# Performance work log

Hardware: AMD Instinct MI355X
Metric: run time of the kernel (lower is better)

Reference implementation:

```python
import jax, jax.numpy as jnp
import numpy as np
import math

B, T, F_ = 4, 1024, 1024
TO_DIM, FROM_DIM, LATENT, H = 1024, 1024, 1024, 16
HEAD_DIM = LATENT // H

def _linear_params(key, in_dim, out_dim):
    kw, kb = jax.random.split(key)
    bound = 1.0 / math.sqrt(in_dim)
    W = jax.random.uniform(kw, (out_dim, in_dim), minval=-bound, maxval=bound, dtype=jnp.float32)
    b = jax.random.uniform(kb, (out_dim,), minval=-bound, maxval=bound, dtype=jnp.float32)
    return W, b

def setup_inputs() -> dict:
    key = jax.random.key(0)
    ks = jax.random.split(key, 7)
    X_to = jax.random.normal(ks[0], (B, T, TO_DIM), dtype=jnp.float32)
    X_from = jax.random.normal(ks[1], (B, F_, FROM_DIM), dtype=jnp.float32)
    mask_from = jax.random.randint(ks[2], (B, T, F_), 0, 2, dtype=jnp.int32)
    Wq, bq = _linear_params(ks[3], TO_DIM, LATENT)
    Wk, bk = _linear_params(ks[4], FROM_DIM, LATENT)
    Wv, bv = _linear_params(ks[5], FROM_DIM, LATENT)
    Wo, bo = _linear_params(ks[6], LATENT, TO_DIM)
    return {"X_to": X_to, "X_from": X_from, "mask_from": mask_from,
            "Wq": Wq, "bq": bq, "Wk": Wk, "bk": bk, "Wv": Wv, "bv": bv, "Wo": Wo, "bo": bo}

def _split_heads(x):
    # [b, t, (h k)] -> [b, h, t, k]
    b, t, _ = x.shape
    return x.reshape(b, t, H, HEAD_DIM).transpose(0, 2, 1, 3)

def reference(X_to, X_from, mask_from, Wq, bq, Wk, bk, Wv, bv, Wo, bo):
    Q = _split_heads(X_to @ Wq.T + bq)
    # NOTE: source swaps names — K comes from v_linear, V from k_linear. Reproduced literally.
    K = _split_heads(X_from @ Wv.T + bv)
    V = _split_heads(X_from @ Wk.T + bk)
    attn = jnp.einsum('bhtk,bhfk->bhtf', Q, K) / math.sqrt(HEAD_DIM)
    attn = jnp.where(mask_from[:, None, :, :] == 0, jnp.float32(-10000.0), attn)
    attn = jax.nn.softmax(attn, axis=-1)
    out = jnp.einsum('bhtf,bhfk->bhtk', attn, V)  # [b,h,t,k]
    out = out.transpose(0, 2, 1, 3).reshape(X_to.shape[0], X_to.shape[1], LATENT)
    return out @ Wo.T + bo
```

## Files before the change

### kernel.cpp

```cpp
#include <hip/hip_runtime.h>
#include <hip/hip_bf16.h>
#include <math.h>

#define BB 4
#define TT 1024
#define FF 1024
#define DIM 1024
#define NH 16
#define HD 64
#define MROWS (BB * TT)
#define FB (FF / 64)

typedef __attribute__((ext_vector_type(8))) short short8;
typedef __attribute__((ext_vector_type(4))) float f32x4;
typedef __hip_bfloat16 bf16;

__device__ __forceinline__ void async_copy16(const void* g, void* l) {
    __builtin_amdgcn_global_load_lds((const __attribute__((address_space(1))) void*)g,
                                     (__attribute__((address_space(3))) void*)l,
                                     16, 0, 0);
}

struct ConvArgs {
    const float* src[6];
    bf16* dst[6];
    int nvec[6];
    int blk_end[6];
};

__global__ __launch_bounds__(256) void convert_batch(ConvArgs a) {
    int bx = blockIdx.x;
    int seg = 0;
#pragma unroll
    for (int k = 0; k < 5; ++k) if (bx >= a.blk_end[k]) seg = k + 1;
    int b0 = seg ? a.blk_end[seg - 1] : 0;
    int idx = (bx - b0) * 256 + threadIdx.x;
    if (idx >= a.nvec[seg]) return;
    float4 v = ((const float4*)a.src[seg])[idx];
    union { bf16 t[4]; ushort4 u; } o;
    o.t[0] = __float2bfloat16(v.x);
    o.t[1] = __float2bfloat16(v.y);
    o.t[2] = __float2bfloat16(v.z);
    o.t[3] = __float2bfloat16(v.w);
    *(ushort4*)(a.dst[seg] + 4 * (size_t)idx) = o.u;
}

__global__ __launch_bounds__(256) void mask_pack(const int* __restrict__ mask,
                                                 unsigned long long* __restrict__ Mb) {
    const int lane = threadIdx.x & 63;
    const int w = (blockIdx.x * 256 + threadIdx.x) >> 6;
    const int nw = (gridDim.x * 256) >> 6;
    const int NCH = BB * TT * FB;
    for (int c = w; c < NCH; c += nw) {
        int v = mask[(size_t)c * 64 + lane];
        unsigned long long bits = __ballot(v != 0);
        if (lane == 0) Mb[c] = bits;
    }
}

struct QkvArgs {
    const bf16* A[3]; const bf16* W[3]; const float* bias[3]; bf16* C[3];
    int N[3]; int biasRow[3];
};

__global__ __launch_bounds__(256) void gemm_qkv(QkvArgs q) {
    __shared__ bf16 As[128 * 32];
    __shared__ bf16 Bs[128 * 32];

    const int op = blockIdx.z;
    const bf16* A = q.A[op];
    const bf16* W = q.W[op];
    const float* bias = q.bias[op];
    bf16* C = q.C[op];
    const int N = q.N[op];
    const int brow = q.biasRow[op];

    int m0, n0;
    if (brow) { m0 = blockIdx.x * 128; n0 = blockIdx.y * 128; }
    else      { n0 = blockIdx.x * 128; m0 = blockIdx.y * 128; }

    const int tid  = threadIdx.x;
    const int lane = tid & 63;
    const int wave = tid >> 6;
    const int quad = lane >> 4;
    const int l16  = lane & 15;
    const int wm = wave & 1;
    const int wn = wave >> 1;
    const int wbase = tid & ~63;

    f32x4 acc[4][4] = {};

    for (int k0 = 0; k0 < DIM; k0 += 32) {
#pragma unroll
        for (int j = 0; j < 2; ++j) {
            int slot = j * 256 + tid;
            int r = slot >> 2;
            int blk = (slot & 3) ^ (r & 3);
            async_copy16(A + (size_t)(m0 + r) * DIM + k0 + blk * 8,
                         As + (size_t)(j * 256 + wbase) * 8);
            async_copy16(W + (size_t)(n0 + r) * DIM + k0 + blk * 8,
                         Bs + (size_t)(j * 256 + wbase) * 8);
        }
        __syncthreads();

        short8 a[4], b[4];
#pragma unroll
        for (int mi = 0; mi < 4; ++mi) {
            int r = wm * 64 + mi * 16 + l16;
            a[mi] = *(const short8*)(As + r * 32 + ((quad ^ (r & 3)) * 8));
        }
#pragma unroll
        for (int ni = 0; ni < 4; ++ni) {
            int r = wn * 64 + ni * 16 + l16;
            b[ni] = *(const short8*)(Bs + r * 32 + ((quad ^ (r & 3)) * 8));
        }
#pragma unroll
        for (int mi = 0; mi < 4; ++mi)
#pragma unroll
            for (int ni = 0; ni < 4; ++ni)
                acc[mi][ni] = __builtin_amdgcn_mfma_f32_16x16x32_bf16(
                    a[mi], b[ni], acc[mi][ni], 0, 0, 0);
        __syncthreads();
    }

#pragma unroll
    for (int ni = 0; ni < 4; ++ni) {
        const int n = n0 + wn * 64 + ni * 16 + l16;
        float bcol = brow ? 0.0f : bias[n];
#pragma unroll
        for (int mi = 0; mi < 4; ++mi) {
#pragma unroll
            for (int i = 0; i < 4; ++i) {
                const int m = m0 + wm * 64 + mi * 16 + quad * 4 + i;
                float v = acc[mi][ni][i] + (brow ? bias[m] : bcol);
                C[(size_t)m * N + n] = __float2bfloat16(v);
            }
        }
    }
}

__global__ __launch_bounds__(256) void gemm_o(
    const bf16* __restrict__ A, const bf16* __restrict__ W,
    const float* __restrict__ bias, float* __restrict__ C)
{
    __shared__ bf16 As[128 * 32];
    __shared__ bf16 Bs[64 * 32];

    const int n0 = blockIdx.x * 64;
    const int m0 = blockIdx.y * 128;
    const int tid  = threadIdx.x;
    const int lane = tid & 63;
    const int wave = tid >> 6;
    const int quad = lane >> 4;
    const int l16  = lane & 15;
    const int wm = wave & 1;
    const int wn = wave >> 1;
    const int wbase = tid & ~63;

    f32x4 acc[4][2] = {};

    for (int k0 = 0; k0 < DIM; k0 += 32) {
#pragma unroll
        for (int j = 0; j < 2; ++j) {
            int slot = j * 256 + tid;
            int r = slot >> 2;
            int blk = (slot & 3) ^ (r & 3);
            async_copy16(A + (size_t)(m0 + r) * DIM + k0 + blk * 8,
                         As + (size_t)(j * 256 + wbase) * 8);
        }
        {
            int r = tid >> 2;
            int blk = (tid & 3) ^ (r & 3);
            async_copy16(W + (size_t)(n0 + r) * DIM + k0 + blk * 8,
                         Bs + (size_t)wbase * 8);
        }
        __syncthreads();

        short8 a[4], b[2];
#pragma unroll
        for (int mi = 0; mi < 4; ++mi) {
            int r = wm * 64 + mi * 16 + l16;
            a[mi] = *(const short8*)(As + r * 32 + ((quad ^ (r & 3)) * 8));
        }
#pragma unroll
        for (int ni = 0; ni < 2; ++ni) {
            int r = wn * 32 + ni * 16 + l16;
            b[ni] = *(const short8*)(Bs + r * 32 + ((quad ^ (r & 3)) * 8));
        }
#pragma unroll
        for (int mi = 0; mi < 4; ++mi)
#pragma unroll
            for (int ni = 0; ni < 2; ++ni)
                acc[mi][ni] = __builtin_amdgcn_mfma_f32_16x16x32_bf16(
                    a[mi], b[ni], acc[mi][ni], 0, 0, 0);
        __syncthreads();
    }

#pragma unroll
    for (int ni = 0; ni < 2; ++ni) {
        const int n = n0 + wn * 32 + ni * 16 + l16;
        const float bcol = bias[n];
#pragma unroll
        for (int mi = 0; mi < 4; ++mi)
#pragma unroll
            for (int i = 0; i < 4; ++i) {
                const int m = m0 + wm * 64 + mi * 16 + quad * 4 + i;
                C[(size_t)m * DIM + n] = acc[mi][ni][i] + bcol;
            }
    }
}

__global__ __launch_bounds__(256) void attn_kernel(
    const bf16* Qg, const bf16* __restrict__ Kg, const bf16* __restrict__ Vtg,
    const unsigned long long* __restrict__ Mbits, bf16* Og)
{
    __shared__ bf16 Ks[64 * 64];
    __shared__ bf16 Vts[64 * 64];
    __shared__ bf16 Ps[64 * 72];

    const int tid  = threadIdx.x;
    const int lane = tid & 63;
    const int wave = tid >> 6;
    const int quad = lane >> 4;
    const int l16  = lane & 15;
    const int t0 = blockIdx.x * 64;
    const int h  = blockIdx.y;
    const int b  = blockIdx.z;
    const size_t qrow0 = (size_t)b * TT + t0;
    const size_t krow0 = (size_t)b * FF;
    const int wbase = tid & ~63;

    const bf16* qptr = Qg + (qrow0 + wave * 16 + l16) * DIM + h * HD;
    short8 qa0 = *(const short8*)(qptr + quad * 8);
    short8 qa1 = *(const short8*)(qptr + 32 + quad * 8);

    float lrow[4] = {0.f, 0.f, 0.f, 0.f};
    f32x4 oacc[4] = {};

    for (int f0 = 0; f0 < FF; f0 += 64) {
        const int fb = f0 >> 6;
#pragma unroll
        for (int j = 0; j < 2; ++j) {
            int slot = j * 256 + tid;
            int r = slot >> 3;
            int blk = (slot & 7) ^ (r & 7);
            async_copy16(Kg + (krow0 + f0 + r) * DIM + h * HD + blk * 8,
                         Ks + (size_t)(j * 256 + wbase) * 8);
            async_copy16(Vtg + (size_t)(h * HD + r) * MROWS + b * FF + f0 + blk * 8,
                         Vts + (size_t)(j * 256 + wbase) * 8);
        }
        __syncthreads();

        f32x4 sacc[4] = {};
#pragma unroll
        for (int nt = 0; nt < 4; ++nt) {
            int r = nt * 16 + l16;
            short8 kb0 = *(const short8*)(Ks + r * 64 + ((quad       ^ (r & 7)) * 8));
            short8 kb1 = *(const short8*)(Ks + r * 64 + (((quad + 4) ^ (r & 7)) * 8));
            sacc[nt] = __builtin_amdgcn_mfma_f32_16x16x32_bf16(qa0, kb0, sacc[nt], 0, 0, 0);
            sacc[nt] = __builtin_amdgcn_mfma_f32_16x16x32_bf16(qa1, kb1, sacc[nt], 0, 0, 0);
        }

#pragma unroll
        for (int i = 0; i < 4; ++i) {
            const int prow = wave * 16 + quad * 4 + i;
            unsigned long long m64 = Mbits[(qrow0 + prow) * FB + fb];
            unsigned long long sh = m64 >> l16;
            unsigned lo = (unsigned)sh, hi = (unsigned)(sh >> 32);
            float p0 = (lo & 1u)         ? __expf(sacc[0][i] * 0.125f) : 0.f;
            float p1 = ((lo >> 16) & 1u) ? __expf(sacc[1][i] * 0.125f) : 0.f;
            float p2 = (hi & 1u)         ? __expf(sacc[2][i] * 0.125f) : 0.f;
            float p3 = ((hi >> 16) & 1u) ? __expf(sacc[3][i] * 0.125f) : 0.f;
            lrow[i] += p0 + p1 + p2 + p3;
            Ps[prow * 72 +  0 + l16] = __float2bfloat16(p0);
            Ps[prow * 72 + 16 + l16] = __float2bfloat16(p1);
            Ps[prow * 72 + 32 + l16] = __float2bfloat16(p2);
            Ps[prow * 72 + 48 + l16] = __float2bfloat16(p3);
        }

        short8 pa0 = *(const short8*)(Ps + (wave * 16 + l16) * 72 + quad * 8);
        short8 pa1 = *(const short8*)(Ps + (wave * 16 + l16) * 72 + 32 + quad * 8);
#pragma unroll
        for (int nt = 0; nt < 4; ++nt) {
            int r = nt * 16 + l16;
            short8 vb0 = *(const short8*)(Vts + r * 64 + ((quad       ^ (r & 7)) * 8));
            short8 vb1 = *(const short8*)(Vts + r * 64 + (((quad + 4) ^ (r & 7)) * 8));
            oacc[nt] = __builtin_amdgcn_mfma_f32_16x16x32_bf16(pa0, vb0, oacc[nt], 0, 0, 0);
            oacc[nt] = __builtin_amdgcn_mfma_f32_16x16x32_bf16(pa1, vb1, oacc[nt], 0, 0, 0);
        }
        __syncthreads();
    }

#pragma unroll
    for (int i = 0; i < 4; ++i) {
        float l = lrow[i];
        l += __shfl_xor(l, 1);
        l += __shfl_xor(l, 2);
        l += __shfl_xor(l, 4);
        l += __shfl_xor(l, 8);
        float inv = 1.0f / l;
        const int prow = wave * 16 + quad * 4 + i;
#pragma unroll
        for (int nt = 0; nt < 4; ++nt)
            Ps[prow * 72 + nt * 16 + l16] = __float2bfloat16(oacc[nt][i] * inv);
    }
    __syncthreads();
#pragma unroll
    for (int j = 0; j < 2; ++j) {
        int s = j * 256 + tid;
        int rr = s >> 3, off = (s & 7) * 8;
        short8 v = *(const short8*)(Ps + rr * 72 + off);
        *(short8*)(Og + (qrow0 + rr) * DIM + h * HD + off) = v;
    }
}

extern "C" void kernel_launch(void* const* d_in, const int* in_sizes, int n_in,
                              void* d_out, int out_size, void* d_ws, size_t ws_size,
                              hipStream_t stream) {
    const float* X_to   = (const float*)d_in[0];
    const float* X_from = (const float*)d_in[1];
    const int*   mask   = (const int*)  d_in[2];
    const float* Wq     = (const float*)d_in[3];
    const float* bq     = (const float*)d_in[4];
    const float* Wk     = (const float*)d_in[5];
    const float* bk     = (const float*)d_in[6];
    const float* Wv     = (const float*)d_in[7];
    const float* bv     = (const float*)d_in[8];
    const float* Wo     = (const float*)d_in[9];
    const float* bo     = (const float*)d_in[10];
    float* out = (float*)d_out;

    char* ws = (char*)d_ws;
    bf16* Xt16 = (bf16*)(ws);
    bf16* Xf16 = (bf16*)(ws + (8u  << 20));
    bf16* Wq16 = (bf16*)(ws + (16u << 20));
    bf16* Wv16 = (bf16*)(ws + (18u << 20));
    bf16* Wk16 = (bf16*)(ws + (20u << 20));
    bf16* Wo16 = (bf16*)(ws + (22u << 20));
    bf16* Q16  = (bf16*)(ws + (24u << 20));
    bf16* K16  = (bf16*)(ws + (32u << 20));
    bf16* Vt16 = (bf16*)(ws + (40u << 20));
    unsigned long long* Mb = (unsigned long long*)(ws + (48u << 20));

    ConvArgs ca;
    ca.src[0] = X_to;   ca.dst[0] = Xt16; ca.nvec[0] = MROWS * DIM / 4;
    ca.src[1] = X_from; ca.dst[1] = Xf16; ca.nvec[1] = MROWS * DIM / 4;
    ca.src[2] = Wq;     ca.dst[2] = Wq16; ca.nvec[2] = DIM * DIM / 4;
    ca.src[3] = Wv;     ca.dst[3] = Wv16; ca.nvec[3] = DIM * DIM / 4;
    ca.src[4] = Wk;     ca.dst[4] = Wk16; ca.nvec[4] = DIM * DIM / 4;
    ca.src[5] = Wo;     ca.dst[5] = Wo16; ca.nvec[5] = DIM * DIM / 4;
    int cum = 0;
    for (int k = 0; k < 6; ++k) { cum += ca.nvec[k] / 256; ca.blk_end[k] = cum; }
    convert_batch<<<cum, 256, 0, stream>>>(ca);

    mask_pack<<<256, 256, 0, stream>>>(mask, Mb);

    QkvArgs qa;
    qa.A[0] = Xt16; qa.W[0] = Wq16; qa.bias[0] = bq; qa.C[0] = Q16;
    qa.N[0] = DIM; qa.biasRow[0] = 0;
    qa.A[1] = Xf16; qa.W[1] = Wv16; qa.bias[1] = bv; qa.C[1] = K16;
    qa.N[1] = DIM; qa.biasRow[1] = 0;
    qa.A[2] = Wk16; qa.W[2] = Xf16; qa.bias[2] = bk; qa.C[2] = Vt16;
    qa.N[2] = MROWS; qa.biasRow[2] = 1;
    gemm_qkv<<<dim3(8, 32, 3), 256, 0, stream>>>(qa);

    attn_kernel<<<dim3(TT / 64, NH, BB), 256, 0, stream>>>(
        Q16, K16, Vt16, Mb, Q16);

    gemm_o<<<dim3(DIM / 64, MROWS / 128), 256, 0, stream>>>(Q16, Wo16, bo, out);
}
```

Before: 244.5 us.

## Double GEMM K-tile, stage epilogue through LDS, fuse mask packing into convert

Raises the GEMM K-tile from 32 to 64 with an 8-way XOR swizzle, halving the barrier count per K loop. Both GEMM epilogues write results to padded LDS and then issue 16-byte coalesced global stores instead of scattered scalar stores. Mask bit-packing is merged into the convert kernel as extra blocks to save a launch. Larger LDS use may lower occupancy, and the padded strides leave vector LDS reads only partially aligned.

```diff
diff --git a/kernel.cpp b/kernel.cpp
--- a/kernel.cpp
+++ b/kernel.cpp
@@ -26,10 +26,24 @@
     bf16* dst[6];
     int nvec[6];
     int blk_end[6];
+    const int* mask;
+    unsigned long long* Mb;
 };
 
-__global__ __launch_bounds__(256) void convert_batch(ConvArgs a) {
+__global__ __launch_bounds__(256) void convert_pack(ConvArgs a) {
     int bx = blockIdx.x;
+    if (bx >= a.blk_end[5]) {
+        const int lane = threadIdx.x & 63;
+        const int waveId = (bx - a.blk_end[5]) * 4 + (threadIdx.x >> 6);
+#pragma unroll
+        for (int it = 0; it < 16; ++it) {
+            int c = waveId * 16 + it;
+            int v = a.mask[(size_t)c * 64 + lane];
+            unsigned long long bits = __ballot(v != 0);
+            if (lane == 0) a.Mb[c] = bits;
+        }
+        return;
+    }
     int seg = 0;
 #pragma unroll
     for (int k = 0; k < 5; ++k) if (bx >= a.blk_end[k]) seg = k + 1;
@@ -45,18 +59,7 @@
     *(ushort4*)(a.dst[seg] + 4 * (size_t)idx) = o.u;
 }
 
-__global__ __launch_bounds__(256) void mask_pack(const int* __restrict__ mask,
-                                                 unsigned long long* __restrict__ Mb) {
-    const int lane = threadIdx.x & 63;
-    const int w = (blockIdx.x * 256 + threadIdx.x) >> 6;
-    const int nw = (gridDim.x * 256) >> 6;
-    const int NCH = BB * TT * FB;
-    for (int c = w; c < NCH; c += nw) {
-        int v = mask[(size_t)c * 64 + lane];
-        unsigned long long bits = __ballot(v != 0);
-        if (lane == 0) Mb[c] = bits;
-    }
-}
+#define BK 64
 
 struct QkvArgs {
     const bf16* A[3]; const bf16* W[3]; const float* bias[3]; bf16* C[3];
@@ -64,8 +67,9 @@
 };
 
 __global__ __launch_bounds__(256) void gemm_qkv(QkvArgs q) {
-    __shared__ bf16 As[128 * 32];
-    __shared__ bf16 Bs[128 * 32];
+    __shared__ bf16 smem[128 * 132];
+    bf16* As = smem;
+    bf16* Bs = smem + 128 * BK;
 
     const int op = blockIdx.z;
     const bf16* A = q.A[op];
@@ -90,52 +94,65 @@
 
     f32x4 acc[4][4] = {};
 
-    for (int k0 = 0; k0 < DIM; k0 += 32) {
-#pragma unroll
-        for (int j = 0; j < 2; ++j) {
+    for (int k0 = 0; k0 < DIM; k0 += BK) {
+#pragma unroll
+        for (int j = 0; j < 4; ++j) {
             int slot = j * 256 + tid;
-            int r = slot >> 2;
-            int blk = (slot & 3) ^ (r & 3);
-            async_copy16(A + (size_t)(m0 + r) * DIM + k0 + blk * 8,
+            int r = slot >> 3;
+            int g = (slot & 7) ^ (r & 7);
+            async_copy16(A + (size_t)(m0 + r) * DIM + k0 + g * 8,
                          As + (size_t)(j * 256 + wbase) * 8);
-            async_copy16(W + (size_t)(n0 + r) * DIM + k0 + blk * 8,
+            async_copy16(W + (size_t)(n0 + r) * DIM + k0 + g * 8,
                          Bs + (size_t)(j * 256 + wbase) * 8);
         }
         __syncthreads();
 
-        short8 a[4], b[4];
-#pragma unroll
-        for (int mi = 0; mi < 4; ++mi) {
-            int r = wm * 64 + mi * 16 + l16;
-            a[mi] = *(const short8*)(As + r * 32 + ((quad ^ (r & 3)) * 8));
-        }
-#pragma unroll
-        for (int ni = 0; ni < 4; ++ni) {
-            int r = wn * 64 + ni * 16 + l16;
-            b[ni] = *(const short8*)(Bs + r * 32 + ((quad ^ (r & 3)) * 8));
-        }
+#pragma unroll
+        for (int kk = 0; kk < 2; ++kk) {
+            short8 a[4], b[4];
+#pragma unroll
+            for (int mi = 0; mi < 4; ++mi) {
+                int r = wm * 64 + mi * 16 + l16;
+                int p = (kk * 4 + quad) ^ (r & 7);
+                a[mi] = *(const short8*)(As + r * BK + p * 8);
+            }
+#pragma unroll
+            for (int ni = 0; ni < 4; ++ni) {
+                int r = wn * 64 + ni * 16 + l16;
+                int p = (kk * 4 + quad) ^ (r & 7);
+                b[ni] = *(const short8*)(Bs + r * BK + p * 8);
+            }
+#pragma unroll
+            for (int mi = 0; mi < 4; ++mi)
+#pragma unroll
+                for (int ni = 0; ni < 4; ++ni)
+                    acc[mi][ni] = __builtin_amdgcn_mfma_f32_16x16x32_bf16(
+                        a[mi], b[ni], acc[mi][ni], 0, 0, 0);
+        }
+        __syncthreads();
+    }
+
+    bf16* Cs = smem;
+#pragma unroll
+    for (int ni = 0; ni < 4; ++ni) {
+        const int nl = wn * 64 + ni * 16 + l16;
+        float bcol = brow ? 0.0f : bias[n0 + nl];
 #pragma unroll
         for (int mi = 0; mi < 4; ++mi)
 #pragma unroll
-            for (int ni = 0; ni < 4; ++ni)
-                acc[mi][ni] = __builtin_amdgcn_mfma_f32_16x16x32_bf16(
-                    a[mi], b[ni], acc[mi][ni], 0, 0, 0);
-        __syncthreads();
-    }
-
-#pragma unroll
-    for (int ni = 0; ni < 4; ++ni) {
-        const int n = n0 + wn * 64 + ni * 16 + l16;
-        float bcol = brow ? 0.0f : bias[n];
-#pragma unroll
-        for (int mi = 0; mi < 4; ++mi) {
-#pragma unroll
             for (int i = 0; i < 4; ++i) {
-                const int m = m0 + wm * 64 + mi * 16 + quad * 4 + i;
-                float v = acc[mi][ni][i] + (brow ? bias[m] : bcol);
-                C[(size_t)m * N + n] = __float2bfloat16(v);
-            }
-        }
+                const int ml = wm * 64 + mi * 16 + quad * 4 + i;
+                float v = acc[mi][ni][i] + (brow ? bias[m0 + ml] : bcol);
+                Cs[ml * 132 + nl] = __float2bfloat16(v);
+            }
+    }
+    __syncthreads();
+#pragma unroll
+    for (int j = 0; j < 8; ++j) {
+        int slot = j * 256 + tid;
+        int rr = slot >> 4, cc = slot & 15;
+        short8 v = *(const short8*)(Cs + rr * 132 + cc * 8);
+        *(short8*)(C + (size_t)(m0 + rr) * N + n0 + cc * 8) = v;
     }
 }
 
@@ -143,8 +160,9 @@
     const bf16* __restrict__ A, const bf16* __restrict__ W,
     const float* __restrict__ bias, float* __restrict__ C)
 {
-    __shared__ bf16 As[128 * 32];
-    __shared__ bf16 Bs[64 * 32];
+    __shared__ float smemf[128 * 66];
+    bf16* As = (bf16*)smemf;
+    bf16* Bs = As + 128 * BK;
 
     const int n0 = blockIdx.x * 64;
     const int m0 = blockIdx.y * 128;
@@ -159,54 +177,70 @@
 
     f32x4 acc[4][2] = {};
 
-    for (int k0 = 0; k0 < DIM; k0 += 32) {
+    for (int k0 = 0; k0 < DIM; k0 += BK) {
+#pragma unroll
+        for (int j = 0; j < 4; ++j) {
+            int slot = j * 256 + tid;
+            int r = slot >> 3;
+            int g = (slot & 7) ^ (r & 7);
+            async_copy16(A + (size_t)(m0 + r) * DIM + k0 + g * 8,
+                         As + (size_t)(j * 256 + wbase) * 8);
+        }
 #pragma unroll
         for (int j = 0; j < 2; ++j) {
             int slot = j * 256 + tid;
-            int r = slot >> 2;
-            int blk = (slot & 3) ^ (r & 3);
-            async_copy16(A + (size_t)(m0 + r) * DIM + k0 + blk * 8,
-                         As + (size_t)(j * 256 + wbase) * 8);
-        }
-        {
-            int r = tid >> 2;
-            int blk = (tid & 3) ^ (r & 3);
-            async_copy16(W + (size_t)(n0 + r) * DIM + k0 + blk * 8,
-                         Bs + (size_t)wbase * 8);
-        }
-        __syncthreads();
-
-        short8 a[4], b[2];
-#pragma unroll
-        for (int mi = 0; mi < 4; ++mi) {
-            int r = wm * 64 + mi * 16 + l16;
-            a[mi] = *(const short8*)(As + r * 32 + ((quad ^ (r & 3)) * 8));
-        }
-#pragma unroll
-        for (int ni = 0; ni < 2; ++ni) {
-            int r = wn * 32 + ni * 16 + l16;
-            b[ni] = *(const short8*)(Bs + r * 32 + ((quad ^ (r & 3)) * 8));
-        }
+            int r = slot >> 3;
+            int g = (slot & 7) ^ (r & 7);
+            async_copy16(W + (size_t)(n0 + r) * DIM + k0 + g * 8,
+                         Bs + (size_t)(j * 256 + wbase) * 8);
+        }
+        __syncthreads();
+
+#pragma unroll
+        for (int kk = 0; kk < 2; ++kk) {
+            short8 a[4], b[2];
+#pragma unroll
+            for (int mi = 0; mi < 4; ++mi) {
+                int r = wm * 64 + mi * 16 + l16;
+                int p = (kk * 4 + quad) ^ (r & 7);
+                a[mi] = *(const short8*)(As + r * BK + p * 8);
+            }
+#pragma unroll
+            for (int ni = 0; ni < 2; ++ni) {
+                int r = wn * 32 + ni * 16 + l16;
+                int p = (kk * 4 + quad) ^ (r & 7);
+                b[ni] = *(const short8*)(Bs + r * BK + p * 8);
+            }
+#pragma unroll
+            for (int mi = 0; mi < 4; ++mi)
+#pragma unroll
+                for (int ni = 0; ni < 2; ++ni)
+                    acc[mi][ni] = __builtin_amdgcn_mfma_f32_16x16x32_bf16(
+                        a[mi], b[ni], acc[mi][ni], 0, 0, 0);
+        }
+        __syncthreads();
+    }
+
+    float* Cs = smemf;
+#pragma unroll
+    for (int ni = 0; ni < 2; ++ni) {
+        const int nl = wn * 32 + ni * 16 + l16;
+        const float bcol = bias[n0 + nl];
 #pragma unroll
         for (int mi = 0; mi < 4; ++mi)
 #pragma unroll
-            for (int ni = 0; ni < 2; ++ni)
-                acc[mi][ni] = __builtin_amdgcn_mfma_f32_16x16x32_bf16(
-                    a[mi], b[ni], acc[mi][ni], 0, 0, 0);
-        __syncthreads();
-    }
-
-#pragma unroll
-    for (int ni = 0; ni < 2; ++ni) {
-        const int n = n0 + wn * 32 + ni * 16 + l16;
-        const float bcol = bias[n];
-#pragma unroll
-        for (int mi = 0; mi < 4; ++mi)
-#pragma unroll
             for (int i = 0; i < 4; ++i) {
-                const int m = m0 + wm * 64 + mi * 16 + quad * 4 + i;
-                C[(size_t)m * DIM + n] = acc[mi][ni][i] + bcol;
-            }
+                const int ml = wm * 64 + mi * 16 + quad * 4 + i;
+                Cs[ml * 66 + nl] = acc[mi][ni][i] + bcol;
+            }
+    }
+    __syncthreads();
+#pragma unroll
+    for (int j = 0; j < 8; ++j) {
+        int slot = j * 256 + tid;
+        int rr = slot >> 4, cc = slot & 15;
+        float4 v = *(const float4*)(Cs + rr * 66 + cc * 4);
+        *(float4*)(C + (size_t)(m0 + rr) * DIM + n0 + cc * 4) = v;
     }
 }
 
@@ -351,9 +385,8 @@
     ca.src[5] = Wo;     ca.dst[5] = Wo16; ca.nvec[5] = DIM * DIM / 4;
     int cum = 0;
     for (int k = 0; k < 6; ++k) { cum += ca.nvec[k] / 256; ca.blk_end[k] = cum; }
-    convert_batch<<<cum, 256, 0, stream>>>(ca);
-
-    mask_pack<<<256, 256, 0, stream>>>(mask, Mb);
+    ca.mask = mask; ca.Mb = Mb;
+    convert_pack<<<cum + 1024, 256, 0, stream>>>(ca);
 
     QkvArgs qa;
     qa.A[0] = Xt16; qa.W[0] = Wq16; qa.bias[0] = bq; qa.C[0] = Q16;
```

After: 233.6 us. 1.05x faster.
